# Kernel tuning notes

Measured on AMD Instinct MI355X. Metric: run time of the kernel, lower is better.

## Reference

```python
import jax, jax.numpy as jnp
import numpy as np

H, DH = 8, 40            # heads, dim_head -> inner_dim = 320
SCALE = DH ** -0.5
B, N, M = 16, 4096, 77   # batch, query tokens (64x64 latent), text tokens
QD, CD, ID = 320, 768, H * DH


def setup_inputs() -> dict:
    key = jax.random.key(0)
    ks = jax.random.split(key, 7)
    x = jax.random.normal(ks[0], (B, N, QD), dtype=jnp.float32)
    context = jax.random.normal(ks[1], (B, M, CD), dtype=jnp.float32)
    # Linear weights stored as (in, out); torch nn.Linear has no bias for q/k/v
    Wq = jax.random.normal(ks[2], (QD, ID), dtype=jnp.float32) * (QD ** -0.5)
    Wk = jax.random.normal(ks[3], (CD, ID), dtype=jnp.float32) * (CD ** -0.5)
    Wv = jax.random.normal(ks[4], (CD, ID), dtype=jnp.float32) * (CD ** -0.5)
    Wo = jax.random.normal(ks[5], (ID, QD), dtype=jnp.float32) * (ID ** -0.5)
    bo = jnp.zeros((QD,), dtype=jnp.float32)
    return {"x": x, "context": context, "Wq": Wq, "Wk": Wk, "Wv": Wv, "Wo": Wo, "bo": bo}


def reference(x, context, Wq, Wk, Wv, Wo, bo):
    b, n, _ = x.shape
    m = context.shape[1]
    q = (x @ Wq).reshape(b, n, H, DH)        # to_q
    k = (context @ Wk).reshape(b, m, H, DH)  # to_k
    v = (context @ Wv).reshape(b, m, H, DH)  # to_v
    # full QK^T * scale (rank-bias path inactive: rank={} / is_add_rank=False)
    scores = jnp.einsum('bihd,bjhd->bhij', q, k) * SCALE  # [B,H,N,M]
    attn = jax.nn.softmax(scores, axis=-1)
    out = jnp.einsum('bhij,bjhd->bihd', attn, v).reshape(b, n, ID)
    return out @ Wo + bo  # to_out Linear; Dropout(p=0.0) is identity
```

## Files before the change

kernel.cpp:

```cpp
#include <hip/hip_runtime.h>

typedef unsigned short u16;
using short8 = __attribute__((ext_vector_type(8))) short;
using f32x4  = __attribute__((ext_vector_type(4))) float;

#define SCALE 0.15811388300841897f

__device__ __forceinline__ u16 f2bf(float f) {
  unsigned int u = __float_as_uint(f);
  u += 0x7fffu + ((u >> 16) & 1u);
  return (u16)(u >> 16);
}


__global__ void prep_transpose(const float* __restrict__ Wq, const float* __restrict__ Wo,
                               const float* __restrict__ Wk, const float* __restrict__ Wv,
                               u16* __restrict__ wqt, u16* __restrict__ wot,
                               u16* __restrict__ wkt, u16* __restrict__ wvt) {
  __shared__ float ld[64][65];
  const int bid = blockIdx.x;
  const float* src; u16* dst; int K; float scale; int tk, tn;
  if (bid < 25)       { src = Wq; dst = wqt; K = 320; scale = SCALE; tk = bid / 5;         tn = bid % 5; }
  else if (bid < 50)  { src = Wo; dst = wot; K = 320; scale = 1.f;   tk = (bid - 25) / 5;  tn = (bid - 25) % 5; }
  else if (bid < 110) { src = Wk; dst = wkt; K = 768; scale = 1.f;   tk = (bid - 50) / 5;  tn = (bid - 50) % 5; }
  else                { src = Wv; dst = wvt; K = 768; scale = 1.f;   tk = (bid - 110) / 5; tn = (bid - 110) % 5; }
  const int c = threadIdx.x & 63, r0 = threadIdx.x >> 6;
  for (int rr = r0; rr < 64; rr += 4)
    ld[rr][c] = src[(size_t)(tk * 64 + rr) * 320 + tn * 64 + c];
  __syncthreads();
  for (int rr = r0; rr < 64; rr += 4)
    dst[(size_t)(tn * 64 + rr) * K + tk * 64 + c] = f2bf(ld[c][rr] * scale);
}

__global__ __launch_bounds__(512, 1)
void kv_mfma(const float* __restrict__ ctx,
             const u16* __restrict__ wkt, const u16* __restrict__ wvt,
             u16* __restrict__ kbf, u16* __restrict__ vt) {
  const int b = blockIdx.x;
  const int tid = threadIdx.x;
  const int w = tid >> 6, l = tid & 63, l16 = l & 15, lhi = l >> 4;
  __shared__ __align__(16) u16 sctx[80][776];

  for (int i = tid; i < 80 * 192; i += 512) {
    int row = i / 192, c4 = (i - row * 192) * 4;
    ushort4 u;
    if (row < 77) {
      float4 v = *reinterpret_cast<const float4*>(&ctx[(size_t)(b * 77 + row) * 768 + c4]);
      u.x = f2bf(v.x); u.y = f2bf(v.y); u.z = f2bf(v.z); u.w = f2bf(v.w);
    } else u = (ushort4){0, 0, 0, 0};
    *reinterpret_cast<ushort4*>(&sctx[row][c4]) = u;
  }
  for (int i = tid; i < 8 * 80 * 3; i += 512) {
    int hm = i / 3, q = i - hm * 3;
    int h = hm / 80, m = hm - h * 80;
    *reinterpret_cast<uint4*>(&kbf[(((size_t)b * 8 + h) * 80 + m) * 64 + 40 + q * 8]) = (uint4){0, 0, 0, 0};
  }
  for (int i = tid; i < 8 * 48 * 2; i += 512) {
    int hd = i / 2, q = i - hd * 2;
    int h = hd / 48, d = hd - h * 48;
    *reinterpret_cast<uint4*>(&vt[(((size_t)b * 8 + h) * 48 + d) * 96 + 80 + q * 8]) = (uint4){0, 0, 0, 0};
  }
  for (int i = tid; i < 8 * 8 * 10; i += 512) {
    int h = i / 80, rem = i - h * 80;
    int d = 40 + rem / 10, q = rem - (rem / 10) * 10;
    *reinterpret_cast<uint4*>(&vt[(((size_t)b * 8 + h) * 48 + d) * 96 + q * 8]) = (uint4){0, 0, 0, 0};
  }
  __syncthreads();

  f32x4 acc[5][5];
  #pragma unroll
  for (int rt = 0; rt < 5; ++rt)
    #pragma unroll
    for (int nt = 0; nt < 5; ++nt) acc[rt][nt] = (f32x4){0.f, 0.f, 0.f, 0.f};

  const u16* wbase = (w < 4) ? (wkt + (size_t)(w * 80) * 768)
                             : (wvt + (size_t)((w - 4) * 80) * 768);
  #pragma unroll 2
  for (int ks = 0; ks < 24; ++ks) {
    short8 af[5];
    #pragma unroll
    for (int rt = 0; rt < 5; ++rt)
      af[rt] = *reinterpret_cast<const short8*>(&sctx[rt * 16 + l16][ks * 32 + lhi * 8]);
    short8 bf[5];
    #pragma unroll
    for (int nt = 0; nt < 5; ++nt)
      bf[nt] = *reinterpret_cast<const short8*>(&wbase[(size_t)(nt * 16 + l16) * 768 + ks * 32 + lhi * 8]);
    #pragma unroll
    for (int rt = 0; rt < 5; ++rt)
      #pragma unroll
      for (int nt = 0; nt < 5; ++nt)
        acc[rt][nt] = __builtin_amdgcn_mfma_f32_16x16x32_bf16(af[rt], bf[nt], acc[rt][nt], 0, 0, 0);
  }

  if (w < 4) {
    #pragma unroll
    for (int rt = 0; rt < 5; ++rt)
      #pragma unroll
      for (int nt = 0; nt < 5; ++nt) {
        int c = w * 80 + nt * 16 + l16, h = c / 40, d = c - h * 40;
        #pragma unroll
        for (int r = 0; r < 4; ++r) {
          int m = rt * 16 + lhi * 4 + r;
          kbf[(((size_t)b * 8 + h) * 80 + m) * 64 + d] = f2bf(m < 77 ? acc[rt][nt][r] : 0.f);
        }
      }
  } else {
    #pragma unroll
    for (int rt = 0; rt < 5; ++rt)
      #pragma unroll
      for (int nt = 0; nt < 5; ++nt) {
        int c = (w - 4) * 80 + nt * 16 + l16, h = c / 40, d = c - h * 40;
        #pragma unroll
        for (int r = 0; r < 4; ++r) {
          int m = rt * 16 + lhi * 4 + r;
          vt[(((size_t)b * 8 + h) * 48 + d) * 96 + m] = f2bf(m < 77 ? acc[rt][nt][r] : 0.f);
        }
      }
  }
}

__global__ __launch_bounds__(256, 3)
void qproj(const float* __restrict__ x, const u16* __restrict__ wqt,
           u16* __restrict__ qg) {
  const int tid = threadIdx.x;
  const int w = tid >> 6, l = tid & 63, l16 = l & 15, lhi = l >> 4;
  const int r0 = blockIdx.x * 64;
  __shared__ __align__(16) u16 xs[64][328];

  const float4* xin = reinterpret_cast<const float4*>(x + (size_t)r0 * 320);
  for (int i = tid; i < 64 * 80; i += 256) {
    float4 v = xin[i];
    int row = i / 80, c4 = (i - row * 80) * 4;
    ushort4 u;
    u.x = f2bf(v.x); u.y = f2bf(v.y); u.z = f2bf(v.z); u.w = f2bf(v.w);
    *reinterpret_cast<ushort4*>(&xs[row][c4]) = u;
  }
  if (blockIdx.x == 1023 && tid < 64) qg[(size_t)65536 * 320 + tid] = 0;
  __syncthreads();

  f32x4 acc[4][5];
  #pragma unroll
  for (int rt = 0; rt < 4; ++rt)
    #pragma unroll
    for (int nt = 0; nt < 5; ++nt) acc[rt][nt] = (f32x4){0.f, 0.f, 0.f, 0.f};
  #pragma unroll 2
  for (int ks = 0; ks < 10; ++ks) {
    short8 af[4];
    #pragma unroll
    for (int rt = 0; rt < 4; ++rt)
      af[rt] = *reinterpret_cast<const short8*>(&xs[rt * 16 + l16][ks * 32 + lhi * 8]);
    #pragma unroll
    for (int nt = 0; nt < 5; ++nt) {
      short8 bf = *reinterpret_cast<const short8*>(&wqt[(size_t)(w * 80 + nt * 16 + l16) * 320 + ks * 32 + lhi * 8]);
      #pragma unroll
      for (int rt = 0; rt < 4; ++rt)
        acc[rt][nt] = __builtin_amdgcn_mfma_f32_16x16x32_bf16(af[rt], bf, acc[rt][nt], 0, 0, 0);
    }
  }
  #pragma unroll
  for (int rt = 0; rt < 4; ++rt)
    #pragma unroll
    for (int nt = 0; nt < 5; ++nt) {
      int col = w * 80 + nt * 16 + l16;
      #pragma unroll
      for (int r = 0; r < 4; ++r) {
        int row = rt * 16 + lhi * 4 + r;
        qg[(size_t)(r0 + row) * 320 + col] = f2bf(acc[rt][nt][r]);
      }
    }
}

__global__ __launch_bounds__(512, 4)
void attn3(const u16* __restrict__ qg, const u16* __restrict__ kbf,
           const u16* __restrict__ vtp, const u16* __restrict__ wot,
           const float* __restrict__ bo, float* __restrict__ out) {
  const int b  = blockIdx.y;
  const int q0 = blockIdx.x * 64;
  const int tid = threadIdx.x;
  const int w   = tid >> 6;
  const int l   = tid & 63;
  const int l16 = l & 15;
  const int lhi = l >> 4;
  const int wq  = w & 3;
  const int hg  = w >> 2;

  __shared__ __align__(16) u16 XO[64][328];
  __shared__ __align__(16) u16 Pt[8][16][104];

  if (l < 32) {
    int r = l >> 1, q = l & 1;
    *reinterpret_cast<uint4*>(&Pt[w][r][80 + 8 * q]) = (uint4){0u, 0u, 0u, 0u};
  }

  for (int hi = 0; hi < 4; ++hi) {
    const int h = hg * 4 + hi;
    const u16* kh = kbf + ((size_t)(b * 8 + h)) * 80 * 64;
    const u16* vh = vtp + ((size_t)(b * 8 + h)) * 48 * 96;
    f32x4 sacc[5];
    #pragma unroll
    for (int mt = 0; mt < 5; ++mt) sacc[mt] = (f32x4){0.f, 0.f, 0.f, 0.f};
    #pragma unroll
    for (int ks = 0; ks < 2; ++ks) {
      short8 a = *reinterpret_cast<const short8*>(
          &qg[(size_t)(b * 4096 + q0 + wq * 16 + l16) * 320 + h * 40 + ks * 32 + lhi * 8]);
      #pragma unroll
      for (int mt = 0; mt < 5; ++mt) {
        short8 bb = *reinterpret_cast<const short8*>(&kh[(mt * 16 + l16) * 64 + ks * 32 + lhi * 8]);
        sacc[mt] = __builtin_amdgcn_mfma_f32_16x16x32_bf16(a, bb, sacc[mt], 0, 0, 0);
      }
    }
    #pragma unroll
    for (int r = 0; r < 4; ++r) {
      float sv[5];
      float mx = -1e30f;
      #pragma unroll
      for (int mt = 0; mt < 5; ++mt) {
        float s = sacc[mt][r];
        if (mt * 16 + l16 >= 77) s = -1e30f;
        sv[mt] = s;
        mx = fmaxf(mx, s);
      }
      mx = fmaxf(mx, __shfl_xor(mx, 1));
      mx = fmaxf(mx, __shfl_xor(mx, 2));
      mx = fmaxf(mx, __shfl_xor(mx, 4));
      mx = fmaxf(mx, __shfl_xor(mx, 8));
      float sum = 0.f;
      #pragma unroll
      for (int mt = 0; mt < 5; ++mt) { sv[mt] = __expf(sv[mt] - mx); sum += sv[mt]; }
      sum += __shfl_xor(sum, 1);
      sum += __shfl_xor(sum, 2);
      sum += __shfl_xor(sum, 4);
      sum += __shfl_xor(sum, 8);
      float rs = 1.f / sum;
      int row = lhi * 4 + r;
      #pragma unroll
      for (int mt = 0; mt < 5; ++mt)
        Pt[w][row][mt * 16 + l16] = f2bf(sv[mt] * rs);
    }
    asm volatile("s_waitcnt lgkmcnt(0)" ::: "memory");
    __builtin_amdgcn_sched_barrier(0);
    f32x4 oacc[3];
    #pragma unroll
    for (int nt = 0; nt < 3; ++nt) oacc[nt] = (f32x4){0.f, 0.f, 0.f, 0.f};
    #pragma unroll
    for (int ks = 0; ks < 3; ++ks) {
      short8 a = *reinterpret_cast<const short8*>(&Pt[w][l16][ks * 32 + lhi * 8]);
      #pragma unroll
      for (int nt = 0; nt < 3; ++nt) {
        short8 bb = *reinterpret_cast<const short8*>(&vh[(nt * 16 + l16) * 96 + ks * 32 + lhi * 8]);
        oacc[nt] = __builtin_amdgcn_mfma_f32_16x16x32_bf16(a, bb, oacc[nt], 0, 0, 0);
      }
    }
    #pragma unroll
    for (int nt = 0; nt < 3; ++nt) {
      int d = nt * 16 + l16;
      if (d < 40) {
        #pragma unroll
        for (int r = 0; r < 4; ++r)
          XO[wq * 16 + lhi * 4 + r][h * 40 + d] = f2bf(oacc[nt][r]);
      }
    }
  }
  __syncthreads();

  {
    const int w2 = w >> 2, w4 = w & 3;
    f32x4 cacc[2][5];
    #pragma unroll
    for (int rt = 0; rt < 2; ++rt)
      #pragma unroll
      for (int nt = 0; nt < 5; ++nt) cacc[rt][nt] = (f32x4){0.f, 0.f, 0.f, 0.f};
    #pragma unroll 2
    for (int ks = 0; ks < 10; ++ks) {
      short8 af[2];
      #pragma unroll
      for (int rt = 0; rt < 2; ++rt)
        af[rt] = *reinterpret_cast<const short8*>(&XO[w2 * 32 + rt * 16 + l16][ks * 32 + lhi * 8]);
      #pragma unroll
      for (int nt = 0; nt < 5; ++nt) {
        short8 bf = *reinterpret_cast<const short8*>(&wot[(size_t)(w4 * 80 + nt * 16 + l16) * 320 + ks * 32 + lhi * 8]);
        #pragma unroll
        for (int rt = 0; rt < 2; ++rt)
          cacc[rt][nt] = __builtin_amdgcn_mfma_f32_16x16x32_bf16(af[rt], bf, cacc[rt][nt], 0, 0, 0);
      }
    }
    #pragma unroll
    for (int nt = 0; nt < 5; ++nt) {
      int col = w4 * 80 + nt * 16 + l16;
      float bias = bo[col];
      #pragma unroll
      for (int rt = 0; rt < 2; ++rt) {
        #pragma unroll
        for (int r = 0; r < 4; ++r) {
          int row = w2 * 32 + rt * 16 + lhi * 4 + r;
          out[(size_t)(b * 4096 + q0 + row) * 320 + col] = cacc[rt][nt][r] + bias;
        }
      }
    }
  }
}

extern "C" void kernel_launch(void* const* d_in, const int* in_sizes, int n_in,
                              void* d_out, int out_size, void* d_ws, size_t ws_size,
                              hipStream_t stream) {
  (void)in_sizes; (void)n_in; (void)out_size; (void)ws_size;
  const float* x       = (const float*)d_in[0];
  const float* context = (const float*)d_in[1];
  const float* Wq      = (const float*)d_in[2];
  const float* Wk      = (const float*)d_in[3];
  const float* Wv      = (const float*)d_in[4];
  const float* Wo      = (const float*)d_in[5];
  const float* bo      = (const float*)d_in[6];
  float* out = (float*)d_out;
  u16* ws = (u16*)d_ws;
  u16* wqt = ws;
  u16* wot = ws + 102400;
  u16* wkt = ws + 204800;
  u16* wvt = ws + 450560;
  u16* kbf = ws + 696320;
  u16* vtp = ws + 1351680;
  u16* qg  = ws + 1941504;

  prep_transpose<<<170, 256, 0, stream>>>(Wq, Wo, Wk, Wv, wqt, wot, wkt, wvt);
  kv_mfma<<<16, 512, 0, stream>>>(context, wkt, wvt, kbf, vtp);
  qproj<<<1024, 256, 0, stream>>>(x, wqt, qg);
  attn3<<<dim3(64, 16), 512, 0, stream>>>(qg, kbf, vtp, wot, bo, out);
}
```

Before: 208.7 us.

## Split fused attention+out-projection into separate attention and out-proj kernels

Breaks the fused attention kernel into two. The attention kernel writes its per-head output back in place into the Q buffer in global memory, and a separate outproj kernel stages those rows in shared memory and multiplies them by Wo. Without the large XO shared buffer, the attention kernel uses less LDS and its launch bounds are raised to allow more resident blocks. The cost is an extra global write and read of the 4096x16x320 bf16 intermediate, plus one more kernel launch.

```diff
diff --git a/kernel.cpp b/kernel.cpp
--- a/kernel.cpp
+++ b/kernel.cpp
@@ -170,10 +170,9 @@
     }
 }
 
-__global__ __launch_bounds__(512, 4)
-void attn3(const u16* __restrict__ qg, const u16* __restrict__ kbf,
-           const u16* __restrict__ vtp, const u16* __restrict__ wot,
-           const float* __restrict__ bo, float* __restrict__ out) {
+__global__ __launch_bounds__(512, 8)
+void attn_sm(u16* __restrict__ qg, const u16* __restrict__ kbf,
+             const u16* __restrict__ vtp) {
   const int b  = blockIdx.y;
   const int q0 = blockIdx.x * 64;
   const int tid = threadIdx.x;
@@ -184,13 +183,14 @@
   const int wq  = w & 3;
   const int hg  = w >> 2;
 
-  __shared__ __align__(16) u16 XO[64][328];
   __shared__ __align__(16) u16 Pt[8][16][104];
 
   if (l < 32) {
     int r = l >> 1, q = l & 1;
     *reinterpret_cast<uint4*>(&Pt[w][r][80 + 8 * q]) = (uint4){0u, 0u, 0u, 0u};
   }
+
+  const size_t rowbase = (size_t)(b * 4096 + q0 + wq * 16);
 
   for (int hi = 0; hi < 4; ++hi) {
     const int h = hg * 4 + hi;
@@ -202,7 +202,7 @@
     #pragma unroll
     for (int ks = 0; ks < 2; ++ks) {
       short8 a = *reinterpret_cast<const short8*>(
-          &qg[(size_t)(b * 4096 + q0 + wq * 16 + l16) * 320 + h * 40 + ks * 32 + lhi * 8]);
+          &qg[(rowbase + l16) * 320 + h * 40 + ks * 32 + lhi * 8]);
       #pragma unroll
       for (int mt = 0; mt < 5; ++mt) {
         short8 bb = *reinterpret_cast<const short8*>(&kh[(mt * 16 + l16) * 64 + ks * 32 + lhi * 8]);
@@ -251,50 +251,64 @@
         oacc[nt] = __builtin_amdgcn_mfma_f32_16x16x32_bf16(a, bb, oacc[nt], 0, 0, 0);
       }
     }
+    asm volatile("s_waitcnt lgkmcnt(0)" ::: "memory");
+    __builtin_amdgcn_sched_barrier(0);
     #pragma unroll
     for (int nt = 0; nt < 3; ++nt) {
       int d = nt * 16 + l16;
       if (d < 40) {
         #pragma unroll
         for (int r = 0; r < 4; ++r)
-          XO[wq * 16 + lhi * 4 + r][h * 40 + d] = f2bf(oacc[nt][r]);
-      }
-    }
+          qg[(rowbase + lhi * 4 + r) * 320 + h * 40 + d] = f2bf(oacc[nt][r]);
+      }
+    }
+  }
+}
+
+__global__ __launch_bounds__(256, 4)
+void outproj(const u16* __restrict__ og, const u16* __restrict__ wot,
+             const float* __restrict__ bo, float* __restrict__ out) {
+  const int tid = threadIdx.x;
+  const int w = tid >> 6, l = tid & 63, l16 = l & 15, lhi = l >> 4;
+  const int r0 = blockIdx.x * 64;
+  __shared__ __align__(16) u16 os[64][328];
+
+  for (int i = tid; i < 64 * 40; i += 256) {
+    int row = i / 40, c8 = (i - row * 40) * 8;
+    *reinterpret_cast<uint4*>(&os[row][c8]) =
+        *reinterpret_cast<const uint4*>(&og[(size_t)(r0 + row) * 320 + c8]);
   }
   __syncthreads();
 
-  {
-    const int w2 = w >> 2, w4 = w & 3;
-    f32x4 cacc[2][5];
-    #pragma unroll
-    for (int rt = 0; rt < 2; ++rt)
-      #pragma unroll
-      for (int nt = 0; nt < 5; ++nt) cacc[rt][nt] = (f32x4){0.f, 0.f, 0.f, 0.f};
-    #pragma unroll 2
-    for (int ks = 0; ks < 10; ++ks) {
-      short8 af[2];
-      #pragma unroll
-      for (int rt = 0; rt < 2; ++rt)
-        af[rt] = *reinterpret_cast<const short8*>(&XO[w2 * 32 + rt * 16 + l16][ks * 32 + lhi * 8]);
-      #pragma unroll
-      for (int nt = 0; nt < 5; ++nt) {
-        short8 bf = *reinterpret_cast<const short8*>(&wot[(size_t)(w4 * 80 + nt * 16 + l16) * 320 + ks * 32 + lhi * 8]);
-        #pragma unroll
-        for (int rt = 0; rt < 2; ++rt)
-          cacc[rt][nt] = __builtin_amdgcn_mfma_f32_16x16x32_bf16(af[rt], bf, cacc[rt][nt], 0, 0, 0);
-      }
-    }
+  f32x4 acc[4][5];
+  #pragma unroll
+  for (int rt = 0; rt < 4; ++rt)
+    #pragma unroll
+    for (int nt = 0; nt < 5; ++nt) acc[rt][nt] = (f32x4){0.f, 0.f, 0.f, 0.f};
+  #pragma unroll 2
+  for (int ks = 0; ks < 10; ++ks) {
+    short8 af[4];
+    #pragma unroll
+    for (int rt = 0; rt < 4; ++rt)
+      af[rt] = *reinterpret_cast<const short8*>(&os[rt * 16 + l16][ks * 32 + lhi * 8]);
     #pragma unroll
     for (int nt = 0; nt < 5; ++nt) {
-      int col = w4 * 80 + nt * 16 + l16;
-      float bias = bo[col];
-      #pragma unroll
-      for (int rt = 0; rt < 2; ++rt) {
-        #pragma unroll
-        for (int r = 0; r < 4; ++r) {
-          int row = w2 * 32 + rt * 16 + lhi * 4 + r;
-          out[(size_t)(b * 4096 + q0 + row) * 320 + col] = cacc[rt][nt][r] + bias;
-        }
+      short8 bf = *reinterpret_cast<const short8*>(&wot[(size_t)(w * 80 + nt * 16 + l16) * 320 + ks * 32 + lhi * 8]);
+      #pragma unroll
+      for (int rt = 0; rt < 4; ++rt)
+        acc[rt][nt] = __builtin_amdgcn_mfma_f32_16x16x32_bf16(af[rt], bf, acc[rt][nt], 0, 0, 0);
+    }
+  }
+  #pragma unroll
+  for (int nt = 0; nt < 5; ++nt) {
+    int col = w * 80 + nt * 16 + l16;
+    float bias = bo[col];
+    #pragma unroll
+    for (int rt = 0; rt < 4; ++rt) {
+      #pragma unroll
+      for (int r = 0; r < 4; ++r) {
+        int row = rt * 16 + lhi * 4 + r;
+        out[(size_t)(r0 + row) * 320 + col] = acc[rt][nt][r] + bias;
       }
     }
   }
@@ -324,5 +338,6 @@
   prep_transpose<<<170, 256, 0, stream>>>(Wq, Wo, Wk, Wv, wqt, wot, wkt, wvt);
   kv_mfma<<<16, 512, 0, stream>>>(context, wkt, wvt, kbf, vtp);
   qproj<<<1024, 256, 0, stream>>>(x, wqt, qg);
-  attn3<<<dim3(64, 16), 512, 0, stream>>>(qg, kbf, vtp, wot, bo, out);
-}
+  attn_sm<<<dim3(64, 16), 512, 0, stream>>>(qg, kbf, vtp);
+  outproj<<<1024, 256, 0, stream>>>(qg, wot, bo, out);
+}
```

After: 210.2 us. Within noise of the previous version (+0.7%).
